# Performance work log

Measured on AMD Instinct MI355X. Metric: run time of the kernel, lower is better.

The kernel has to match this reference:

```python
import jax, jax.numpy as jnp
import numpy as np

N_POINTS = 131072
N_ANCHORS = 2048


def setup_inputs() -> dict:
    key = jax.random.key(0)
    k1, k2, k3, k4 = jax.random.split(key, 4)
    locations3d = jax.random.normal(k1, (N_POINTS, 3), dtype=jnp.float32)
    anchor_locations3d = jax.random.normal(k2, (N_ANCHORS, 3), dtype=jnp.float32)
    anchor_coeffs = jax.random.normal(k3, (N_ANCHORS,), dtype=jnp.float32)
    # per-anchor widths, kept strictly positive in [0.1, 1.0)
    anchor_parameters = jax.random.uniform(k4, (N_ANCHORS,), dtype=jnp.float32) * 0.9 + 0.1
    return {
        "locations3d": locations3d,
        "anchor_locations3d": anchor_locations3d,
        "anchor_coeffs": anchor_coeffs,
        "anchor_parameters": anchor_parameters,
    }


def potential_operator(locations3d, anchor_locations3d, anchor_parameters):
    # Pairwise squared distances via the expanded form (avoids [N,M,3] intermediate):
    x_sq = jnp.sum(locations3d * locations3d, axis=-1, keepdims=True)          # [N,1]
    a_sq = jnp.sum(anchor_locations3d * anchor_locations3d, axis=-1)            # [M]
    cross = locations3d @ anchor_locations3d.T                                  # [N,M]
    sqdist = x_sq + a_sq[None, :] - 2.0 * cross
    sqdist = jnp.maximum(sqdist, 0.0)
    inv_two_w2 = 0.5 / (anchor_parameters * anchor_parameters)                  # [M]
    return jnp.exp(-sqdist * inv_two_w2[None, :])                               # [N,M]


def reference(locations3d, anchor_locations3d, anchor_coeffs, anchor_parameters):
    K = potential_operator(locations3d, anchor_locations3d, anchor_parameters)  # [N,M]
    return K @ anchor_coeffs                                                    # [N]
```

## Files before the change

kernel.cpp:

```cpp
#include <hip/hip_runtime.h>

#define N_POINTS  131072
#define N_ANCHORS 2048
#define CHUNKS    32
#define M_PER     (N_ANCHORS / CHUNKS)
#define THREADS   256
#define PTS       4
#define PT_STRIDE (N_POINTS / PTS)
#define LOG2E     1.4426950408889634f

typedef float v2f __attribute__((ext_vector_type(2)));

struct __align__(16) AnchorLds {
    v2f r0, r1, r2, q, sp, cf;
    v2f pad0, pad1;
};

__global__ __launch_bounds__(256, 8) void linear_potential_main(
    const float* __restrict__ xloc,
    const float* __restrict__ aloc,
    const float* __restrict__ coeffs,
    const float* __restrict__ params,
    float* __restrict__ out)
{
    __shared__ AnchorLds sA[M_PER];

    const int t = threadIdx.x;

    if (t < M_PER) {
        const int m  = blockIdx.y * M_PER + t;
        const float a0 = aloc[3 * m + 0];
        const float a1 = aloc[3 * m + 1];
        const float a2 = aloc[3 * m + 2];
        const float w  = params[m];
        const float sp = -(0.5f * LOG2E) / (w * w);
        const float r0 = -2.0f * sp * a0;
        const float r1 = -2.0f * sp * a1;
        const float r2 = -2.0f * sp * a2;
        const float q  = sp * (a0 * a0 + a1 * a1 + a2 * a2);
        const float cf = coeffs[m];
        sA[t].r0 = (v2f){r0, r0};
        sA[t].r1 = (v2f){r1, r1};
        sA[t].r2 = (v2f){r2, r2};
        sA[t].q  = (v2f){q,  q};
        sA[t].sp = (v2f){sp, sp};
        sA[t].cf = (v2f){cf, cf};
    }
    __syncthreads();

    const int tid = blockIdx.x * THREADS + t;
    const int n0 = tid;
    const int n1 = tid + PT_STRIDE;
    const int n2 = tid + 2 * PT_STRIDE;
    const int n3 = tid + 3 * PT_STRIDE;

    const v2f xa = { xloc[3 * n0 + 0], xloc[3 * n1 + 0] };
    const v2f ya = { xloc[3 * n0 + 1], xloc[3 * n1 + 1] };
    const v2f za = { xloc[3 * n0 + 2], xloc[3 * n1 + 2] };
    const v2f xb = { xloc[3 * n2 + 0], xloc[3 * n3 + 0] };
    const v2f yb = { xloc[3 * n2 + 1], xloc[3 * n3 + 1] };
    const v2f zb = { xloc[3 * n2 + 2], xloc[3 * n3 + 2] };

    const v2f ssa = __builtin_elementwise_fma(xa, xa,
                    __builtin_elementwise_fma(ya, ya, za * za));
    const v2f ssb = __builtin_elementwise_fma(xb, xb,
                    __builtin_elementwise_fma(yb, yb, zb * zb));

    v2f acca = { 0.0f, 0.0f };
    v2f accb = { 0.0f, 0.0f };

    #pragma unroll 8
    for (int mm = 0; mm < M_PER; ++mm) {
        const v2f r0 = sA[mm].r0;
        const v2f r1 = sA[mm].r1;
        const v2f r2 = sA[mm].r2;
        const v2f q  = sA[mm].q;
        const v2f sp = sA[mm].sp;
        const v2f cf = sA[mm].cf;

        v2f arga = __builtin_elementwise_fma(sp, ssa, q);
        arga     = __builtin_elementwise_fma(r0, xa, arga);
        arga     = __builtin_elementwise_fma(r1, ya, arga);
        arga     = __builtin_elementwise_fma(r2, za, arga);

        v2f argb = __builtin_elementwise_fma(sp, ssb, q);
        argb     = __builtin_elementwise_fma(r0, xb, argb);
        argb     = __builtin_elementwise_fma(r1, yb, argb);
        argb     = __builtin_elementwise_fma(r2, zb, argb);

        v2f ea = { __builtin_amdgcn_exp2f(arga.x), __builtin_amdgcn_exp2f(arga.y) };
        v2f eb = { __builtin_amdgcn_exp2f(argb.x), __builtin_amdgcn_exp2f(argb.y) };

        acca = __builtin_elementwise_fma(cf, ea, acca);
        accb = __builtin_elementwise_fma(cf, eb, accb);
    }

    atomicAdd(&out[n0], acca.x);
    atomicAdd(&out[n1], acca.y);
    atomicAdd(&out[n2], accb.x);
    atomicAdd(&out[n3], accb.y);
}

extern "C" void kernel_launch(void* const* d_in, const int* in_sizes, int n_in,
                              void* d_out, int out_size, void* d_ws, size_t ws_size,
                              hipStream_t stream) {
    const float* xloc   = (const float*)d_in[0];
    const float* aloc   = (const float*)d_in[1];
    const float* coeffs = (const float*)d_in[2];
    const float* params = (const float*)d_in[3];
    float* out = (float*)d_out;

    hipMemsetAsync(d_out, 0, N_POINTS * sizeof(float), stream);

    linear_potential_main<<<dim3(N_POINTS / (THREADS * PTS), CHUNKS),
                            dim3(THREADS), 0, stream>>>(
        xloc, aloc, coeffs, params, out);
}
```

Measured before the change: 98.70 us.

## Software-pipeline anchor LDS loads with double-buffered registers and double chunk count

Replaces the unrolled anchor loop with an explicit two-stage register double buffer, so the next anchor's LDS reads are issued while the current anchor's FMAs and exp2 run. Doubles CHUNKS to 64, which halves anchors per block and doubles grid size and atomic traffic. Drops the padded LDS struct for a compact 6-element array. The non-unrolled loop adds a branch and loop overhead per pair of anchors, and the extra blocks add setup and atomics.

```diff
diff --git a/kernel.cpp b/kernel.cpp
--- a/kernel.cpp
+++ b/kernel.cpp
@@ -2,7 +2,7 @@
 
 #define N_POINTS  131072
 #define N_ANCHORS 2048
-#define CHUNKS    32
+#define CHUNKS    64
 #define M_PER     (N_ANCHORS / CHUNKS)
 #define THREADS   256
 #define PTS       4
@@ -11,11 +11,6 @@
 
 typedef float v2f __attribute__((ext_vector_type(2)));
 
-struct __align__(16) AnchorLds {
-    v2f r0, r1, r2, q, sp, cf;
-    v2f pad0, pad1;
-};
-
 __global__ __launch_bounds__(256, 8) void linear_potential_main(
     const float* __restrict__ xloc,
     const float* __restrict__ aloc,
@@ -23,7 +18,7 @@
     const float* __restrict__ params,
     float* __restrict__ out)
 {
-    __shared__ AnchorLds sA[M_PER];
+    __shared__ v2f sA[M_PER][6];
 
     const int t = threadIdx.x;
 
@@ -39,12 +34,12 @@
         const float r2 = -2.0f * sp * a2;
         const float q  = sp * (a0 * a0 + a1 * a1 + a2 * a2);
         const float cf = coeffs[m];
-        sA[t].r0 = (v2f){r0, r0};
-        sA[t].r1 = (v2f){r1, r1};
-        sA[t].r2 = (v2f){r2, r2};
-        sA[t].q  = (v2f){q,  q};
-        sA[t].sp = (v2f){sp, sp};
-        sA[t].cf = (v2f){cf, cf};
+        sA[t][0] = (v2f){r0, r0};
+        sA[t][1] = (v2f){r1, r1};
+        sA[t][2] = (v2f){r2, r2};
+        sA[t][3] = (v2f){q,  q};
+        sA[t][4] = (v2f){sp, sp};
+        sA[t][5] = (v2f){cf, cf};
     }
     __syncthreads();
 
@@ -69,31 +64,40 @@
     v2f acca = { 0.0f, 0.0f };
     v2f accb = { 0.0f, 0.0f };
 
-    #pragma unroll 8
-    for (int mm = 0; mm < M_PER; ++mm) {
-        const v2f r0 = sA[mm].r0;
-        const v2f r1 = sA[mm].r1;
-        const v2f r2 = sA[mm].r2;
-        const v2f q  = sA[mm].q;
-        const v2f sp = sA[mm].sp;
-        const v2f cf = sA[mm].cf;
+    v2f A0 = sA[0][0], A1 = sA[0][1], A2 = sA[0][2],
+        A3 = sA[0][3], A4 = sA[0][4], A5 = sA[0][5];
+    v2f B0, B1, B2, B3, B4, B5;
 
-        v2f arga = __builtin_elementwise_fma(sp, ssa, q);
-        arga     = __builtin_elementwise_fma(r0, xa, arga);
-        arga     = __builtin_elementwise_fma(r1, ya, arga);
-        arga     = __builtin_elementwise_fma(r2, za, arga);
+#define BODY(c0, c1, c2, c3, c4, c5)                                   \
+    do {                                                               \
+        v2f arga = __builtin_elementwise_fma(c4, ssa, c3);             \
+        arga     = __builtin_elementwise_fma(c0, xa, arga);            \
+        arga     = __builtin_elementwise_fma(c1, ya, arga);            \
+        arga     = __builtin_elementwise_fma(c2, za, arga);            \
+        v2f argb = __builtin_elementwise_fma(c4, ssb, c3);             \
+        argb     = __builtin_elementwise_fma(c0, xb, argb);            \
+        argb     = __builtin_elementwise_fma(c1, yb, argb);            \
+        argb     = __builtin_elementwise_fma(c2, zb, argb);            \
+        v2f ea = { __builtin_amdgcn_exp2f(arga.x),                     \
+                   __builtin_amdgcn_exp2f(arga.y) };                   \
+        v2f eb = { __builtin_amdgcn_exp2f(argb.x),                     \
+                   __builtin_amdgcn_exp2f(argb.y) };                   \
+        acca = __builtin_elementwise_fma(c5, ea, acca);                \
+        accb = __builtin_elementwise_fma(c5, eb, accb);                \
+    } while (0)
 
-        v2f argb = __builtin_elementwise_fma(sp, ssb, q);
-        argb     = __builtin_elementwise_fma(r0, xb, argb);
-        argb     = __builtin_elementwise_fma(r1, yb, argb);
-        argb     = __builtin_elementwise_fma(r2, zb, argb);
-
-        v2f ea = { __builtin_amdgcn_exp2f(arga.x), __builtin_amdgcn_exp2f(arga.y) };
-        v2f eb = { __builtin_amdgcn_exp2f(argb.x), __builtin_amdgcn_exp2f(argb.y) };
-
-        acca = __builtin_elementwise_fma(cf, ea, acca);
-        accb = __builtin_elementwise_fma(cf, eb, accb);
+    #pragma unroll 1
+    for (int mm = 0; mm < M_PER; mm += 2) {
+        B0 = sA[mm + 1][0]; B1 = sA[mm + 1][1]; B2 = sA[mm + 1][2];
+        B3 = sA[mm + 1][3]; B4 = sA[mm + 1][4]; B5 = sA[mm + 1][5];
+        BODY(A0, A1, A2, A3, A4, A5);
+        if (mm + 2 < M_PER) {
+            A0 = sA[mm + 2][0]; A1 = sA[mm + 2][1]; A2 = sA[mm + 2][2];
+            A3 = sA[mm + 2][3]; A4 = sA[mm + 2][4]; A5 = sA[mm + 2][5];
+        }
+        BODY(B0, B1, B2, B3, B4, B5);
     }
+#undef BODY
 
     atomicAdd(&out[n0], acca.x);
     atomicAdd(&out[n1], acca.y);
```

Result: slower. 108.0 us (+9.4%).
